# Kernel optimization log

Measured on AMD Instinct MI355X. Metric: run time of the kernel, lower is better.

Reference implementation:

```python
import jax, jax.numpy as jnp
import numpy as np

B, T, D, H, DK = 4, 2048, 1024, 16, 64  # batch, seq, d_model, heads, head_dim (dk==dv)


def setup_inputs() -> dict:
    key = jax.random.key(0)
    ks = jax.random.split(key, 9)
    s = 0.02
    return {
        "q": jax.random.normal(ks[0], (B, T, D), jnp.float32),
        "k": jax.random.normal(ks[1], (B, T, D), jnp.float32),
        "v": jax.random.normal(ks[2], (B, T, D), jnp.float32),
        "attn_mask": jax.random.randint(ks[3], (B, T, T), 0, 2, jnp.int32),
        "Wq": jax.random.normal(ks[4], (D, H * DK), jnp.float32) * s,
        "bq": jnp.zeros((H * DK,), jnp.float32),
        "Wk": jax.random.normal(ks[5], (D, H * DK), jnp.float32) * s,
        "bk": jnp.zeros((H * DK,), jnp.float32),
        "Wv": jax.random.normal(ks[6], (D, H * DK), jnp.float32) * s,
        "bv": jnp.zeros((H * DK,), jnp.float32),
        "Wo": jax.random.normal(ks[7], (H * DK, D), jnp.float32) * s,
        "bo": jnp.zeros((D,), jnp.float32),
        "gamma": jnp.ones((D,), jnp.float32),
        "beta": jnp.zeros((D,), jnp.float32),
    }


def reference(q, k, v, attn_mask, Wq, bq, Wk, bk, Wv, bv, Wo, bo, gamma, beta):
    Bn, Tq, _ = q.shape
    Tk = k.shape[1]
    residual = q
    mask = attn_mask.astype(jnp.float32)  # (B, Tq, Tk), multiplicative

    qh = (q @ Wq + bq).reshape(Bn, Tq, H, DK)
    kh = (k @ Wk + bk).reshape(Bn, Tk, H, DK)
    vh = (v @ Wv + bv).reshape(Bn, Tk, H, DK)

    # NOTE: original applies NO 1/sqrt(d) scaling (temper is computed but unused)
    attn = jnp.einsum("bqhd,bkhd->hbqk", qh, kh)  # (H, B, Tq, Tk)
    attn = attn * mask[None]                      # multiplicative mask
    attn = attn - jnp.max(attn)                   # GLOBAL max subtract (whole tensor)
    attn = jnp.exp(attn) * mask[None]             # re-mask after exp
    attn = attn / (jnp.sum(attn, axis=-1, keepdims=True) + 1e-15)
    # dropout is identity at inference

    out = jnp.einsum("hbqk,bkhd->bqhd", attn, vh).reshape(Bn, Tq, H * DK)
    out = out @ Wo + bo  # (B, Tq, D); dropout identity

    x = out + residual
    mu = jnp.mean(x, axis=-1, keepdims=True)
    var = jnp.mean((x - mu) ** 2, axis=-1, keepdims=True)
    return (x - mu) / jnp.sqrt(var + 1e-5) * gamma + beta
```

## Files before the change

### kernel.cpp

```cpp
#include <hip/hip_runtime.h>
#include <stdint.h>

#define T_ 2048
#define H_ 16

typedef __attribute__((ext_vector_type(8))) short bf16x8;
typedef __attribute__((ext_vector_type(4))) float f32x4;

__device__ __forceinline__ unsigned short f2bf(float x){
  union { float f; uint32_t u; } v; v.f = x;
  uint32_t r = v.u + 0x7FFFu + ((v.u >> 16) & 1u);
  return (unsigned short)(r >> 16);
}

__device__ __forceinline__ unsigned short f2bf_pos(float x){
  union { float f; uint32_t u; } v; v.f = x;
  return (unsigned short)((v.u + 0x8000u) >> 16);
}

__device__ __forceinline__ void g2l16(const void* g, void* l){
  __builtin_amdgcn_global_load_lds(
      (const __attribute__((address_space(1))) void*)g,
      (__attribute__((address_space(3))) void*)l, 16, 0, 0);
}

__global__ __launch_bounds__(256) void cvt3_kernel(
    const float* __restrict__ q, const float* __restrict__ k, const float* __restrict__ v,
    unsigned short* __restrict__ oq, unsigned short* __restrict__ ok, unsigned short* __restrict__ ov){
  const long NG = (long)8*1024*1024/4;
  long g = (long)blockIdx.x*256 + threadIdx.x;
  const float* s; unsigned short* d;
  if (g < NG){ s=q; d=oq; }
  else if (g < 2*NG){ s=k; d=ok; g-=NG; }
  else { s=v; d=ov; g-=2*NG; }
  long i = g*4;
  float4 val = *(const float4*)(s+i);
  ushort4 r;
  r.x=f2bf(val.x); r.y=f2bf(val.y); r.z=f2bf(val.z); r.w=f2bf(val.w);
  *(ushort4*)(d+i) = r;
}

__global__ __launch_bounds__(256) void wt_kernel(
    const float* __restrict__ W0, const float* __restrict__ W1,
    const float* __restrict__ W2, const float* __restrict__ W3,
    unsigned short* __restrict__ out){
  __shared__ unsigned short t[64][72];
  const float* W = (blockIdx.z==0)?W0:(blockIdx.z==1)?W1:(blockIdx.z==2)?W2:W3;
  const float sc = (blockIdx.z==0) ? 1.44269504f : 1.0f;
  unsigned short* o = out + (size_t)blockIdx.z*1024*1024;
  int k0 = blockIdx.x*64, n0 = blockIdx.y*64;
  int tid = threadIdx.x;
  int i = tid>>2, cs = (tid&3)*16;
  const float* src = W + (size_t)(k0+i)*1024 + n0 + cs;
  #pragma unroll
  for (int c=0;c<16;c+=4){
    float4 vv = *(const float4*)(src + c);
    t[i][cs+c+0]=f2bf(vv.x*sc); t[i][cs+c+1]=f2bf(vv.y*sc);
    t[i][cs+c+2]=f2bf(vv.z*sc); t[i][cs+c+3]=f2bf(vv.w*sc);
  }
  __syncthreads();
  int j = tid>>2; int ks = (tid&3)*16;
  __align__(16) unsigned short buf[16];
  #pragma unroll
  for (int c=0;c<16;c++) buf[c] = t[ks+c][j];
  unsigned short* dst = o + (size_t)(n0+j)*1024 + k0 + ks;
  *(uint4*)dst = *(const uint4*)(buf);
  *(uint4*)(dst+8) = *(const uint4*)(buf+8);
}

__global__ __launch_bounds__(256) void pack_mask_kernel(
    const int* __restrict__ mask, unsigned long long* __restrict__ mw){
  int wid = threadIdx.x>>6, lane = threadIdx.x&63;
  long r = (long)blockIdx.x*4 + wid;
  const int* mrow = mask + r*2048;
  unsigned long long* orow = mw + r*32;
  for (int kk=0; kk<32; kk++){
    int vv = mrow[kk*64 + lane];
    unsigned long long bal = __ballot(vv != 0);
    if (lane==0) orow[kk] = bal;
  }
}

template<bool FUSED>
__global__ __launch_bounds__(256,2) void gemm_nt(
    const unsigned short* __restrict__ A,
    const unsigned short* __restrict__ Bt,
    const float* __restrict__ bias,
    const float* __restrict__ resid,
    void* __restrict__ Cout, float bscale){
  __shared__ unsigned short sA[128*64];
  __shared__ unsigned short sB[128*64];
  const int K = 1024;
  int tid = threadIdx.x;
  int wid = tid>>6, lane = tid&63;
  int ln = lane&15, qd = lane>>4;
  int wr = wid>>1, wc = wid&1;
  long m0 = (long)blockIdx.y*128;
  long n0 = (long)blockIdx.x*128;
  f32x4 acc[4][4] = {};
  for (int k0=0; k0<K; k0+=64){
    __syncthreads();
    #pragma unroll
    for (int s=0;s<4;s++){
      int G = s*256 + tid;
      int mm = G>>3, cc = G&7;
      g2l16(A  + (m0+mm)*(long)K + k0 + ((cc^(mm&7))<<3),
            (char*)sA + (size_t)(s*256 + wid*64)*16);
      g2l16(Bt + (n0+mm)*(long)K + k0 + ((cc^(mm&7))<<3),
            (char*)sB + (size_t)(s*256 + wid*64)*16);
    }
    __syncthreads();
    #pragma unroll
    for (int ks=0;ks<2;ks++){
      bf16x8 af[4], bfv[4];
      #pragma unroll
      for (int i=0;i<4;i++){
        int rowa = wr*64 + i*16 + ln;
        af[i]  = *(const bf16x8*)(sA + rowa*64 + (((ks*4+qd)^(rowa&7))<<3));
        int rowb = wc*64 + i*16 + ln;
        bfv[i] = *(const bf16x8*)(sB + rowb*64 + (((ks*4+qd)^(rowb&7))<<3));
      }
      #pragma unroll
      for (int i=0;i<4;i++)
        #pragma unroll
        for (int j=0;j<4;j++)
          acc[i][j] = __builtin_amdgcn_mfma_f32_16x16x32_bf16(af[i], bfv[j], acc[i][j], 0,0,0);
    }
  }
  long gm0 = m0 + wr*64, gn0 = n0 + wc*64;
  #pragma unroll
  for (int j=0;j<4;j++){
    long gn = gn0 + j*16 + ln;
    float bv = bias[gn]*bscale;
    #pragma unroll
    for (int i=0;i<4;i++){
      long gm = gm0 + i*16 + qd*4;
      #pragma unroll
      for (int r=0;r<4;r++){
        float val = acc[i][j][r] + bv;
        if (FUSED){
          ((float*)Cout)[(gm+r)*1024 + gn] = val + resid[(gm+r)*1024 + gn];
        } else {
          ((unsigned short*)Cout)[(gm+r)*1024 + gn] = f2bf(val);
        }
      }
    }
  }
}

__global__ __launch_bounds__(256) void vt_kernel(
    const unsigned short* __restrict__ vh, unsigned short* __restrict__ vt){
  __shared__ unsigned short t[64][72];
  int t0 = blockIdx.x*64;
  int bh = blockIdx.y;
  int b = bh>>4, h = bh&15;
  int tid = threadIdx.x;
  int i = tid>>2, cs=(tid&3)*16;
  const unsigned short* src = vh + ((long)b*T_ + t0 + i)*1024 + h*64 + cs;
  *(bf16x8*)&t[i][cs]   = *(const bf16x8*)(src);
  *(bf16x8*)&t[i][cs+8] = *(const bf16x8*)(src+8);
  __syncthreads();
  int j = tid>>2; int ks=(tid&3)*16;
  __align__(16) unsigned short buf[16];
  #pragma unroll
  for (int c=0;c<16;c++) buf[c] = t[ks+c][j];
  unsigned short* dst = vt + ((long)bh*64 + j)*2048 + t0 + ks;
  *(uint4*)dst = *(const uint4*)buf;
  *(uint4*)(dst+8) = *(const uint4*)(buf+8);
}

__global__ __launch_bounds__(256,4) void attn_kernel(
    const unsigned short* __restrict__ qh,
    const unsigned short* __restrict__ kh,
    const unsigned short* __restrict__ vt,
    const unsigned long long* __restrict__ mw,
    unsigned short* __restrict__ aout){
  __shared__ unsigned short kS[64*64];
  __shared__ unsigned short vS[64*64];
  __shared__ unsigned short pS[4][16][72];
  __shared__ unsigned long long mS[64];
  int tid=threadIdx.x, wid=tid>>6, lane=tid&63;
  int ln=lane&15, qd=lane>>4;
  int q0 = blockIdx.x*64;
  int bh = blockIdx.y, b = bh>>4, h = bh&15;

  const unsigned short* qp = qh + ((long)b*T_ + q0 + wid*16 + ln)*1024 + h*64 + qd*8;
  bf16x8 qf0 = *(const bf16x8*)qp;
  bf16x8 qf1 = *(const bf16x8*)(qp + 32);

  f32x4 oacc[4] = {};
  float lacc[4] = {0.f,0.f,0.f,0.f};

  const unsigned short* khBase = kh + ((long)b*T_)*1024 + h*64;
  const unsigned short* vtBase = vt + ((long)bh*64)*2048;
  const unsigned long long* mwBase = mw + ((long)b*T_ + q0)*32;

  for (int k0=0; k0<T_; k0+=64){
    __syncthreads();
    #pragma unroll
    for (int s=0;s<2;s++){
      int G = s*256 + tid;
      int ii = G>>3, cc = G&7;
      g2l16(khBase + (long)(k0+ii)*1024 + ((cc^(ii&7))<<3),
            (char*)kS + (size_t)(s*256 + wid*64)*16);
      g2l16(vtBase + (long)ii*2048 + k0 + ((cc^(ii&7))<<3),
            (char*)vS + (size_t)(s*256 + wid*64)*16);
    }
    if (tid < 64) mS[tid] = mwBase[(long)tid*32 + (k0>>6)];
    __syncthreads();

    f32x4 sa[4];
    #pragma unroll
    for (int nt=0;nt<4;nt++){
      f32x4 z = {-20.f,-20.f,-20.f,-20.f};
      int row = nt*16 + ln;
      bf16x8 b0 = *(const bf16x8*)(kS + row*64 + (((qd)^(row&7))<<3));
      z = __builtin_amdgcn_mfma_f32_16x16x32_bf16(qf0, b0, z, 0,0,0);
      bf16x8 b1 = *(const bf16x8*)(kS + row*64 + (((4+qd)^(row&7))<<3));
      z = __builtin_amdgcn_mfma_f32_16x16x32_bf16(qf1, b1, z, 0,0,0);
      sa[nt]=z;
    }

    #pragma unroll
    for (int r=0;r<4;r++){
      unsigned long long bits = mS[wid*16 + qd*4 + r] >> ln;
      #pragma unroll
      for (int nt=0;nt<4;nt++){
        float e = __builtin_amdgcn_exp2f(sa[nt][r]);
        float p = ((bits >> (nt*16)) & 1ULL) ? e : 0.f;
        lacc[r] += p;
        pS[wid][qd*4+r][nt*16+ln] = f2bf_pos(p);
      }
    }
    asm volatile("s_waitcnt lgkmcnt(0)" ::: "memory");

    #pragma unroll
    for (int ks=0;ks<2;ks++){
      bf16x8 pa = *(const bf16x8*)(&pS[wid][ln][ks*32+qd*8]);
      #pragma unroll
      for (int d=0;d<4;d++){
        int row = d*16+ln;
        bf16x8 vb = *(const bf16x8*)(vS + row*64 + (((ks*4+qd)^(row&7))<<3));
        oacc[d] = __builtin_amdgcn_mfma_f32_16x16x32_bf16(pa, vb, oacc[d], 0,0,0);
      }
    }
  }

  #pragma unroll
  for (int off=1; off<16; off<<=1){
    #pragma unroll
    for (int r=0;r<4;r++) lacc[r] += __shfl_xor(lacc[r], off, 64);
  }
  float linv[4];
  #pragma unroll
  for (int r=0;r<4;r++) linv[r] = (lacc[r]>0.f)?(1.f/lacc[r]):0.f;
  long orow = (long)b*T_ + q0 + wid*16 + qd*4;
  #pragma unroll
  for (int d=0;d<4;d++)
    #pragma unroll
    for (int r=0;r<4;r++)
      aout[(orow+r)*1024 + h*64 + d*16 + ln] = f2bf(oacc[d][r]*linv[r]);
}

__global__ __launch_bounds__(256) void ln_kernel(const float* __restrict__ x,
    const float* __restrict__ gamma, const float* __restrict__ beta, float* __restrict__ out){
  __shared__ float red[8];
  long row = blockIdx.x;
  const float* xr = x + row*1024;
  int tid = threadIdx.x;
  float4 v = *(const float4*)(xr + tid*4);
  float s = v.x+v.y+v.z+v.w;
  float sq = v.x*v.x+v.y*v.y+v.z*v.z+v.w*v.w;
  #pragma unroll
  for (int off=1; off<64; off<<=1){
    s  += __shfl_xor(s,off,64);
    sq += __shfl_xor(sq,off,64);
  }
  int wid=tid>>6, lane=tid&63;
  if (lane==0){ red[wid]=s; red[4+wid]=sq; }
  __syncthreads();
  float S  = red[0]+red[1]+red[2]+red[3];
  float SQ = red[4]+red[5]+red[6]+red[7];
  float mu = S*(1.0f/1024.0f);
  float var = SQ*(1.0f/1024.0f) - mu*mu;
  float rstd = rsqrtf(var + 1e-5f);
  float4 g  = *(const float4*)(gamma + tid*4);
  float4 be = *(const float4*)(beta + tid*4);
  float4 o;
  o.x=(v.x-mu)*rstd*g.x+be.x;
  o.y=(v.y-mu)*rstd*g.y+be.y;
  o.z=(v.z-mu)*rstd*g.z+be.z;
  o.w=(v.w-mu)*rstd*g.w+be.w;
  *(float4*)(out + row*1024 + tid*4) = o;
}

extern "C" void kernel_launch(void* const* d_in, const int* in_sizes, int n_in,
                              void* d_out, int out_size, void* d_ws, size_t ws_size,
                              hipStream_t stream){
  const float* q = (const float*)d_in[0];
  const float* k = (const float*)d_in[1];
  const float* v = (const float*)d_in[2];
  const int*   mask = (const int*)d_in[3];
  const float* Wq = (const float*)d_in[4];
  const float* bq = (const float*)d_in[5];
  const float* Wk = (const float*)d_in[6];
  const float* bk = (const float*)d_in[7];
  const float* Wv = (const float*)d_in[8];
  const float* bv = (const float*)d_in[9];
  const float* Wo = (const float*)d_in[10];
  const float* bo = (const float*)d_in[11];
  const float* gamma = (const float*)d_in[12];
  const float* beta  = (const float*)d_in[13];
  float* out = (float*)d_out;
  char* ws = (char*)d_ws;
  const size_t MB = 1024*1024;
  unsigned short*     Wt  = (unsigned short*)(ws + 0);
  unsigned long long* mw  = (unsigned long long*)(ws + 8*MB);
  unsigned short*     qhB = (unsigned short*)(ws + 10*MB);
  unsigned short*     khB = (unsigned short*)(ws + 26*MB);
  unsigned short*     vtB = (unsigned short*)(ws + 42*MB);
  unsigned short*     qbf = (unsigned short*)(ws + 58*MB);
  unsigned short*     kbf = (unsigned short*)(ws + 74*MB);
  unsigned short*     vbf = (unsigned short*)(ws + 90*MB);
  unsigned short*     vhB  = qbf;
  unsigned short*     aout = vbf;
  float*              xbuf = (float*)(ws + 10*MB);

  cvt3_kernel<<<24576,256,0,stream>>>(q,k,v,qbf,kbf,vbf);
  wt_kernel<<<dim3(16,16,4),256,0,stream>>>(Wq,Wk,Wv,Wo,Wt);
  pack_mask_kernel<<<2048,256,0,stream>>>(mask, mw);
  gemm_nt<false><<<dim3(8,64),256,0,stream>>>(qbf, Wt,             bq, nullptr, qhB, 1.44269504f);
  gemm_nt<false><<<dim3(8,64),256,0,stream>>>(kbf, Wt+1024*1024,   bk, nullptr, khB, 1.0f);
  gemm_nt<false><<<dim3(8,64),256,0,stream>>>(vbf, Wt+2*1024*1024, bv, nullptr, vhB, 1.0f);
  vt_kernel<<<dim3(32,64),256,0,stream>>>(vhB, vtB);
  attn_kernel<<<dim3(32,64),256,0,stream>>>(qhB, khB, vtB, mw, aout);
  gemm_nt<true><<<dim3(8,64),256,0,stream>>>(aout, Wt+3*1024*1024, bo, q, xbuf, 1.0f);
  ln_kernel<<<8192,256,0,stream>>>(xbuf, gamma, beta, out);
}
```

Before: 489.8 us.

## Restructure attention to 64 rows per wave and batch the QKV projections

The attention kernel now uses 128-thread blocks where each wave handles 64 query rows, so K fragments loaded from LDS are reused across four row groups. The mask is applied as a large negative bias inside exp2 instead of a select. Row sums are computed with an MFMA against a vector of ones, and P is stored with a permuted column order that vt_kernel matches with a key permutation. The three Q/K/V GEMMs are merged into one launch over grid z. The cost is higher register pressure and fewer blocks per CU, in exchange for fewer LDS reads and less scalar work per MFMA.

```diff
diff --git a/kernel.cpp b/kernel.cpp
--- a/kernel.cpp
+++ b/kernel.cpp
@@ -11,11 +11,6 @@
   union { float f; uint32_t u; } v; v.f = x;
   uint32_t r = v.u + 0x7FFFu + ((v.u >> 16) & 1u);
   return (unsigned short)(r >> 16);
-}
-
-__device__ __forceinline__ unsigned short f2bf_pos(float x){
-  union { float f; uint32_t u; } v; v.f = x;
-  return (unsigned short)((v.u + 0x8000u) >> 16);
 }
 
 __device__ __forceinline__ void g2l16(const void* g, void* l){
@@ -81,15 +76,14 @@
   }
 }
 
-template<bool FUSED>
-__global__ __launch_bounds__(256,2) void gemm_nt(
+template<int FUSED>
+__device__ __forceinline__ void gemm_body(
     const unsigned short* __restrict__ A,
     const unsigned short* __restrict__ Bt,
-    const float* __restrict__ bias,
+    const float* __restrict__ bias, float bscale,
     const float* __restrict__ resid,
-    void* __restrict__ Cout, float bscale){
-  __shared__ unsigned short sA[128*64];
-  __shared__ unsigned short sB[128*64];
+    void* __restrict__ Cout,
+    unsigned short* sA, unsigned short* sB){
   const int K = 1024;
   int tid = threadIdx.x;
   int wid = tid>>6, lane = tid&63;
@@ -105,9 +99,9 @@
       int G = s*256 + tid;
       int mm = G>>3, cc = G&7;
       g2l16(A  + (m0+mm)*(long)K + k0 + ((cc^(mm&7))<<3),
-            (char*)sA + (size_t)(s*256 + wid*64)*16);
+            (char*)sA + (size_t)G*16);
       g2l16(Bt + (n0+mm)*(long)K + k0 + ((cc^(mm&7))<<3),
-            (char*)sB + (size_t)(s*256 + wid*64)*16);
+            (char*)sB + (size_t)G*16);
     }
     __syncthreads();
     #pragma unroll
@@ -146,6 +140,32 @@
       }
     }
   }
+}
+
+__global__ __launch_bounds__(256,2) void gemm_qkv(
+    const unsigned short* __restrict__ Aq, const unsigned short* __restrict__ Ak,
+    const unsigned short* __restrict__ Av, const unsigned short* __restrict__ Wt,
+    const float* __restrict__ bq, const float* __restrict__ bk, const float* __restrict__ bv,
+    unsigned short* __restrict__ Cq, unsigned short* __restrict__ Ck,
+    unsigned short* __restrict__ Cv){
+  __shared__ unsigned short sA[128*64];
+  __shared__ unsigned short sB[128*64];
+  int z = blockIdx.z;
+  const unsigned short* A  = (z==0)?Aq:(z==1)?Ak:Av;
+  const unsigned short* Bt = Wt + (size_t)z*1024*1024;
+  const float* bias        = (z==0)?bq:(z==1)?bk:bv;
+  unsigned short* C        = (z==0)?Cq:(z==1)?Ck:Cv;
+  float bscale             = (z==0)?1.44269504f:1.0f;
+  gemm_body<0>(A, Bt, bias, bscale, nullptr, C, sA, sB);
+}
+
+__global__ __launch_bounds__(256,2) void gemm_out(
+    const unsigned short* __restrict__ A, const unsigned short* __restrict__ Bt,
+    const float* __restrict__ bias, const float* __restrict__ resid,
+    float* __restrict__ Cout){
+  __shared__ unsigned short sA[128*64];
+  __shared__ unsigned short sB[128*64];
+  gemm_body<1>(A, Bt, bias, 1.0f, resid, Cout, sA, sB);
 }
 
 __global__ __launch_bounds__(256) void vt_kernel(
@@ -163,13 +183,17 @@
   int j = tid>>2; int ks=(tid&3)*16;
   __align__(16) unsigned short buf[16];
   #pragma unroll
-  for (int c=0;c<16;c++) buf[c] = t[ks+c][j];
+  for (int c=0;c<16;c++){
+    int p = ks + c;
+    int keyloc = (p&3)*16 + (p>>2);
+    buf[c] = t[keyloc][j];
+  }
   unsigned short* dst = vt + ((long)bh*64 + j)*2048 + t0 + ks;
   *(uint4*)dst = *(const uint4*)buf;
   *(uint4*)(dst+8) = *(const uint4*)(buf+8);
 }
 
-__global__ __launch_bounds__(256,4) void attn_kernel(
+__global__ __launch_bounds__(128,2) void attn_kernel(
     const unsigned short* __restrict__ qh,
     const unsigned short* __restrict__ kh,
     const unsigned short* __restrict__ vt,
@@ -177,89 +201,121 @@
     unsigned short* __restrict__ aout){
   __shared__ unsigned short kS[64*64];
   __shared__ unsigned short vS[64*64];
-  __shared__ unsigned short pS[4][16][72];
-  __shared__ unsigned long long mS[64];
+  __shared__ unsigned short pS[2][64][72];
   int tid=threadIdx.x, wid=tid>>6, lane=tid&63;
   int ln=lane&15, qd=lane>>4;
-  int q0 = blockIdx.x*64;
+  int q0 = blockIdx.x*128;
   int bh = blockIdx.y, b = bh>>4, h = bh&15;
-
-  const unsigned short* qp = qh + ((long)b*T_ + q0 + wid*16 + ln)*1024 + h*64 + qd*8;
-  bf16x8 qf0 = *(const bf16x8*)qp;
-  bf16x8 qf1 = *(const bf16x8*)(qp + 32);
-
-  f32x4 oacc[4] = {};
-  float lacc[4] = {0.f,0.f,0.f,0.f};
-
-  const unsigned short* khBase = kh + ((long)b*T_)*1024 + h*64;
-  const unsigned short* vtBase = vt + ((long)bh*64)*2048;
-  const unsigned long long* mwBase = mw + ((long)b*T_ + q0)*32;
-
-  for (int k0=0; k0<T_; k0+=64){
+  int wq0 = q0 + wid*64;
+
+  bf16x8 qf[4][2];
+  const unsigned short* qbase = qh + ((long)b*T_ + wq0)*1024 + h*64 + qd*8;
+  #pragma unroll
+  for (int rg=0;rg<4;rg++){
+    qf[rg][0] = *(const bf16x8*)(qbase + (size_t)(rg*16+ln)*1024);
+    qf[rg][1] = *(const bf16x8*)(qbase + (size_t)(rg*16+ln)*1024 + 32);
+  }
+  f32x4 oacc[4][4] = {};
+  f32x4 lsum[4] = {};
+  bf16x8 ones;
+  #pragma unroll
+  for (int i=0;i<8;i++) ones[i] = (short)0x3F80;
+
+  const unsigned short* khB  = kh + ((long)b*T_)*1024 + h*64;
+  const unsigned short* vtB2 = vt + ((long)bh*64)*2048;
+  const unsigned long long* mwB = mw + ((long)(b*T_ + wq0 + qd*4))*32;
+
+  for (int t=0; t<32; t++){
     __syncthreads();
     #pragma unroll
-    for (int s=0;s<2;s++){
-      int G = s*256 + tid;
+    for (int s=0;s<4;s++){
+      int G = s*128 + tid;
       int ii = G>>3, cc = G&7;
-      g2l16(khBase + (long)(k0+ii)*1024 + ((cc^(ii&7))<<3),
-            (char*)kS + (size_t)(s*256 + wid*64)*16);
-      g2l16(vtBase + (long)ii*2048 + k0 + ((cc^(ii&7))<<3),
-            (char*)vS + (size_t)(s*256 + wid*64)*16);
-    }
-    if (tid < 64) mS[tid] = mwBase[(long)tid*32 + (k0>>6)];
+      g2l16(khB  + ((long)(t*64+ii))*1024 + ((cc^(ii&7))<<3), (char*)kS + (size_t)G*16);
+      g2l16(vtB2 + (long)ii*2048 + t*64   + ((cc^(ii&7))<<3), (char*)vS + (size_t)G*16);
+    }
+    unsigned long long mb[4][4];
+    #pragma unroll
+    for (int rg=0;rg<4;rg++)
+      #pragma unroll
+      for (int r=0;r<4;r++)
+        mb[rg][r] = mwB[(size_t)(rg*16+r)*32 + t];
     __syncthreads();
 
-    f32x4 sa[4];
-    #pragma unroll
-    for (int nt=0;nt<4;nt++){
-      f32x4 z = {-20.f,-20.f,-20.f,-20.f};
-      int row = nt*16 + ln;
-      bf16x8 b0 = *(const bf16x8*)(kS + row*64 + (((qd)^(row&7))<<3));
-      z = __builtin_amdgcn_mfma_f32_16x16x32_bf16(qf0, b0, z, 0,0,0);
-      bf16x8 b1 = *(const bf16x8*)(kS + row*64 + (((4+qd)^(row&7))<<3));
-      z = __builtin_amdgcn_mfma_f32_16x16x32_bf16(qf1, b1, z, 0,0,0);
-      sa[nt]=z;
-    }
-
-    #pragma unroll
-    for (int r=0;r<4;r++){
-      unsigned long long bits = mS[wid*16 + qd*4 + r] >> ln;
+    bf16x8 kb[2][4];
+    #pragma unroll
+    for (int ks=0;ks<2;ks++)
       #pragma unroll
       for (int nt=0;nt<4;nt++){
-        float e = __builtin_amdgcn_exp2f(sa[nt][r]);
-        float p = ((bits >> (nt*16)) & 1ULL) ? e : 0.f;
-        lacc[r] += p;
-        pS[wid][qd*4+r][nt*16+ln] = f2bf_pos(p);
+        int row = nt*16+ln;
+        kb[ks][nt] = *(const bf16x8*)(kS + row*64 + (((ks*4+qd)^(row&7))<<3));
+      }
+    #pragma unroll
+    for (int rg=0;rg<4;rg++){
+      f32x4 sa[4];
+      #pragma unroll
+      for (int nt=0;nt<4;nt++){
+        f32x4 z = {-20.f,-20.f,-20.f,-20.f};
+        z = __builtin_amdgcn_mfma_f32_16x16x32_bf16(qf[rg][0], kb[0][nt], z, 0,0,0);
+        z = __builtin_amdgcn_mfma_f32_16x16x32_bf16(qf[rg][1], kb[1][nt], z, 0,0,0);
+        sa[nt]=z;
+      }
+      #pragma unroll
+      for (int r=0;r<4;r++){
+        unsigned long long w = mb[rg][r] >> ln;
+        unsigned int lo = (unsigned int)w, hi = (unsigned int)(w>>32);
+        union { uint32_t u; float f; } t0v,t1v,t2v,t3v;
+        t0v.u = ((lo      &1u)-1u) & 0xC47A0000u;
+        t1v.u = (((lo>>16)&1u)-1u) & 0xC47A0000u;
+        t2v.u = ((hi      &1u)-1u) & 0xC47A0000u;
+        t3v.u = (((hi>>16)&1u)-1u) & 0xC47A0000u;
+        float p0 = __builtin_amdgcn_exp2f(sa[0][r] + t0v.f);
+        float p1 = __builtin_amdgcn_exp2f(sa[1][r] + t1v.f);
+        float p2 = __builtin_amdgcn_exp2f(sa[2][r] + t2v.f);
+        float p3 = __builtin_amdgcn_exp2f(sa[3][r] + t3v.f);
+        unsigned a0 = __float_as_uint(p0) + 0x8000u;
+        unsigned a1 = __float_as_uint(p1) + 0x8000u;
+        unsigned a2 = __float_as_uint(p2) + 0x8000u;
+        unsigned a3 = __float_as_uint(p3) + 0x8000u;
+        unsigned loP = __builtin_amdgcn_perm(a1, a0, 0x07060302u);
+        unsigned hiP = __builtin_amdgcn_perm(a3, a2, 0x07060302u);
+        *(unsigned long long*)&pS[wid][rg*16+qd*4+r][ln*4] =
+            ((unsigned long long)hiP<<32) | (unsigned long long)loP;
       }
     }
     asm volatile("s_waitcnt lgkmcnt(0)" ::: "memory");
 
     #pragma unroll
-    for (int ks=0;ks<2;ks++){
-      bf16x8 pa = *(const bf16x8*)(&pS[wid][ln][ks*32+qd*8]);
+    for (int c=0;c<2;c++){
+      bf16x8 vb[4];
       #pragma unroll
       for (int d=0;d<4;d++){
         int row = d*16+ln;
-        bf16x8 vb = *(const bf16x8*)(vS + row*64 + (((ks*4+qd)^(row&7))<<3));
-        oacc[d] = __builtin_amdgcn_mfma_f32_16x16x32_bf16(pa, vb, oacc[d], 0,0,0);
-      }
-    }
-  }
-
-  #pragma unroll
-  for (int off=1; off<16; off<<=1){
-    #pragma unroll
-    for (int r=0;r<4;r++) lacc[r] += __shfl_xor(lacc[r], off, 64);
-  }
-  float linv[4];
-  #pragma unroll
-  for (int r=0;r<4;r++) linv[r] = (lacc[r]>0.f)?(1.f/lacc[r]):0.f;
-  long orow = (long)b*T_ + q0 + wid*16 + qd*4;
-  #pragma unroll
-  for (int d=0;d<4;d++)
-    #pragma unroll
-    for (int r=0;r<4;r++)
-      aout[(orow+r)*1024 + h*64 + d*16 + ln] = f2bf(oacc[d][r]*linv[r]);
+        vb[d] = *(const bf16x8*)(vS + row*64 + (((c*4+qd)^(row&7))<<3));
+      }
+      #pragma unroll
+      for (int rg=0;rg<4;rg++){
+        bf16x8 pa = *(const bf16x8*)&pS[wid][rg*16+ln][c*32+qd*8];
+        #pragma unroll
+        for (int d=0;d<4;d++)
+          oacc[rg][d] = __builtin_amdgcn_mfma_f32_16x16x32_bf16(pa, vb[d], oacc[rg][d], 0,0,0);
+        lsum[rg] = __builtin_amdgcn_mfma_f32_16x16x32_bf16(pa, ones, lsum[rg], 0,0,0);
+      }
+    }
+  }
+
+  #pragma unroll
+  for (int rg=0;rg<4;rg++){
+    float linv[4];
+    #pragma unroll
+    for (int r=0;r<4;r++) linv[r] = (lsum[rg][r]>0.f)?(1.f/lsum[rg][r]):0.f;
+    long rowb = (long)b*T_ + wq0 + rg*16 + qd*4;
+    #pragma unroll
+    for (int d=0;d<4;d++)
+      #pragma unroll
+      for (int r=0;r<4;r++)
+        aout[(rowb+r)*1024 + h*64 + d*16 + ln] = f2bf(oacc[rg][d][r]*linv[r]);
+  }
 }
 
 __global__ __launch_bounds__(256) void ln_kernel(const float* __restrict__ x,
@@ -318,22 +374,20 @@
   unsigned long long* mw  = (unsigned long long*)(ws + 8*MB);
   unsigned short*     qhB = (unsigned short*)(ws + 10*MB);
   unsigned short*     khB = (unsigned short*)(ws + 26*MB);
-  unsigned short*     vtB = (unsigned short*)(ws + 42*MB);
+  unsigned short*     vhB = (unsigned short*)(ws + 42*MB);
   unsigned short*     qbf = (unsigned short*)(ws + 58*MB);
   unsigned short*     kbf = (unsigned short*)(ws + 74*MB);
   unsigned short*     vbf = (unsigned short*)(ws + 90*MB);
-  unsigned short*     vhB  = qbf;
-  unsigned short*     aout = vbf;
+  unsigned short*     vtB  = vbf;
+  unsigned short*     aout = qbf;
   float*              xbuf = (float*)(ws + 10*MB);
 
   cvt3_kernel<<<24576,256,0,stream>>>(q,k,v,qbf,kbf,vbf);
   wt_kernel<<<dim3(16,16,4),256,0,stream>>>(Wq,Wk,Wv,Wo,Wt);
   pack_mask_kernel<<<2048,256,0,stream>>>(mask, mw);
-  gemm_nt<false><<<dim3(8,64),256,0,stream>>>(qbf, Wt,             bq, nullptr, qhB, 1.44269504f);
-  gemm_nt<false><<<dim3(8,64),256,0,stream>>>(kbf, Wt+1024*1024,   bk, nullptr, khB, 1.0f);
-  gemm_nt<false><<<dim3(8,64),256,0,stream>>>(vbf, Wt+2*1024*1024, bv, nullptr, vhB, 1.0f);
+  gemm_qkv<<<dim3(8,64,3),256,0,stream>>>(qbf,kbf,vbf, Wt, bq,bk,bv, qhB,khB,vhB);
   vt_kernel<<<dim3(32,64),256,0,stream>>>(vhB, vtB);
-  attn_kernel<<<dim3(32,64),256,0,stream>>>(qhB, khB, vtB, mw, aout);
-  gemm_nt<true><<<dim3(8,64),256,0,stream>>>(aout, Wt+3*1024*1024, bo, q, xbuf, 1.0f);
+  attn_kernel<<<dim3(16,64),128,0,stream>>>(qhB, khB, vtB, mw, aout);
+  gemm_out<<<dim3(8,64),256,0,stream>>>(aout, Wt+3*1024*1024, bo, q, xbuf);
   ln_kernel<<<8192,256,0,stream>>>(xbuf, gamma, beta, out);
 }
```

After: 477.0 us. -2.6%, faster.
